# Kernel optimization log

Hardware: AMD Instinct MI355X
Metric: run time of the kernel (lower is better)

Reference implementation:

```python
import jax, jax.numpy as jnp
import numpy as np

D_MODEL = 2048; D_STATE = 128; D_CONV = 4; EXPAND = 2
HEADDIM = 64; NGROUPS = 1; CHUNK = 256
D_INNER = EXPAND * D_MODEL          # 4096
NHEADS = D_INNER // HEADDIM         # 64
HG = NHEADS // NGROUPS              # heads per group
CONV_DIM = D_INNER + 2 * NGROUPS * D_STATE          # 4352
D_IN_PROJ = 2 * D_INNER + 2 * NGROUPS * D_STATE + NHEADS  # 8512
BATCH = 2; SEQLEN = 2048
EPS = 1e-5


def setup_inputs() -> dict:
    ks = jax.random.split(jax.random.key(0), 8)
    u = jax.random.normal(ks[0], (BATCH, SEQLEN, D_MODEL), jnp.float32)
    in_proj_w = jax.random.normal(ks[1], (D_IN_PROJ, D_MODEL), jnp.float32) * D_MODEL ** -0.5
    conv_w = jax.random.normal(ks[2], (CONV_DIM, D_CONV), jnp.float32) * D_CONV ** -0.5
    conv_b = jax.random.normal(ks[3], (CONV_DIM,), jnp.float32) * 0.1
    # dt_bias init exactly as in the module: inv softplus of dt ~ U(log(1e-3), log(1e-1))
    dt = jnp.exp(jax.random.uniform(ks[4], (NHEADS,), jnp.float32)
                 * (np.float32(np.log(0.1)) - np.float32(np.log(0.001))) + np.float32(np.log(0.001)))
    dt = jnp.clip(dt, 1e-4, None)
    dt_bias = dt + jnp.log(-jnp.expm1(-dt))
    A_log = jnp.log(jax.random.uniform(ks[5], (NHEADS,), jnp.float32, minval=1.0, maxval=16.0))
    D_skip = jnp.ones((NHEADS,), jnp.float32)
    norm_w = jnp.ones((D_INNER,), jnp.float32)
    out_proj_w = jax.random.normal(ks[6], (D_MODEL, D_INNER), jnp.float32) * D_INNER ** -0.5
    return dict(u=u, in_proj_w=in_proj_w, conv_w=conv_w, conv_b=conv_b,
                dt_bias=dt_bias, A_log=A_log, D_skip=D_skip,
                norm_w=norm_w, out_proj_w=out_proj_w)


def _mamba2(u, in_proj_w, conv_w, conv_b, dt_bias, A_log, D_skip, norm_w, out_proj_w):
    b, l, _ = u.shape
    nc = l // CHUNK
    zxbcdt = u @ in_proj_w.T                                   # (b,l,d_in_proj)
    z = zxbcdt[..., :D_INNER]                                  # gate
    xBC = zxbcdt[..., D_INNER:D_INNER + CONV_DIM]
    dt = jax.nn.softplus(zxbcdt[..., D_INNER + CONV_DIM:] + dt_bias)  # (b,l,h)
    # causal depthwise conv1d (padding d_conv-1, truncated to seqlen) + SiLU
    xp = jnp.pad(xBC, ((0, 0), (D_CONV - 1, 0), (0, 0)))
    conv = conv_b + sum(conv_w[:, k] * xp[:, k:k + l, :] for k in range(D_CONV))
    xBC = jax.nn.silu(conv)
    x = xBC[..., :D_INNER].reshape(b, l, NHEADS, HEADDIM)
    Bm = xBC[..., D_INNER:D_INNER + NGROUPS * D_STATE].reshape(b, l, NGROUPS, D_STATE)
    Cm = xBC[..., D_INNER + NGROUPS * D_STATE:].reshape(b, l, NGROUPS, D_STATE)
    A = -jnp.exp(A_log)                                        # (h,)
    # ---- SSD chunked scan ----
    xc = x.reshape(b, nc, CHUNK, NGROUPS, HG, HEADDIM)         # (b,c,s,g,H,p)
    dtc = dt.reshape(b, nc, CHUNK, NGROUPS, HG)                # (b,c,s,g,H)
    Bc = Bm.reshape(b, nc, CHUNK, NGROUPS, D_STATE)            # (b,c,s,g,n)
    Cc = Cm.reshape(b, nc, CHUNK, NGROUPS, D_STATE)
    dA = jnp.transpose(dtc * A.reshape(NGROUPS, HG), (0, 3, 4, 1, 2))  # (b,g,H,c,s)
    dA_cs = jnp.cumsum(dA, axis=-1)                            # (b,g,H,c,s)
    # intra-chunk: L[i,j] = exp(sum_{j<k<=i} dA_k), lower-triangular (diag=1)
    seg = dA_cs[..., :, None] - dA_cs[..., None, :]            # (b,g,H,c,l,s)
    tri = jnp.tril(jnp.ones((CHUNK, CHUNK), bool))
    Lmat = jnp.where(tri, jnp.exp(seg), 0.0)
    xdt = xc * dtc[..., None]                                  # (b,c,s,g,H,p)
    CB = jnp.einsum('bclgn,bcsgn->bcgls', Cc, Bc)
    Y_diag = jnp.einsum('bcgls,bgHcls,bcsgHp->bclgHp', CB, Lmat, xdt)
    # chunk states and inter-chunk recurrence
    decay_states = jnp.exp(dA_cs[..., -1:] - dA_cs)            # (b,g,H,c,s)
    states = jnp.einsum('bcsgn,bgHcs,bcsgHp->bcgHpn', Bc, decay_states, xdt)
    chunk_decay = jnp.exp(dA_cs[..., -1])                      # (b,g,H,c)

    def step(carry, inp):
        st, dec = inp
        return carry * dec[..., None, None] + st, carry

    _, prev = jax.lax.scan(step, jnp.zeros_like(states[:, 0]),
                           (jnp.moveaxis(states, 1, 0), jnp.moveaxis(chunk_decay, -1, 0)))
    prev = jnp.moveaxis(prev, 0, 1)                            # (b,c,g,H,p,n) state entering chunk
    Y_off = jnp.einsum('bclgn,bcgHpn,bgHcl->bclgHp', Cc, prev, jnp.exp(dA_cs))
    y = (Y_diag + Y_off).reshape(b, l, NHEADS, HEADDIM) + x * D_skip[None, None, :, None]
    y = y.reshape(b, l, D_INNER)
    # gated RMSNorm: gate first (norm_before_gate=False), groupwise rms (ngroups=1 -> full)
    y = y * jax.nn.silu(z)
    yg = y.reshape(b, l, NGROUPS, D_INNER // NGROUPS)
    yg = yg * jax.lax.rsqrt(jnp.mean(yg * yg, axis=-1, keepdims=True) + EPS)
    y = yg.reshape(b, l, D_INNER) * norm_w
    return y @ out_proj_w.T                                    # (b,l,d_model)


def reference(u, in_proj_w, conv_w, conv_b, dt_bias, A_log, D_skip, norm_w, out_proj_w):
    return _mamba2(u, in_proj_w, conv_w, conv_b, dt_bias, A_log, D_skip, norm_w, out_proj_w)
```

## Files before the change

kernel.cpp:

```cpp
#include <hip/hip_runtime.h>
#include <hip/hip_bf16.h>


#define D_MODEL   2048
#define D_STATE   128
#define HEADDIM   64
#define CHUNK     256
#define D_INNER   4096
#define NHEADS    64
#define CONV_DIM  4352
#define D_IN_PROJ 8512
#define SEQLEN    2048
#define NC        8
#define ROWSTOT   4096
#define NPAD      8576
#define RMS_EPS   1e-5f

#define OFF_WIN   0ull
#define OFF_XBF   0ull
#define OFF_PREV  0ull
#define OFF_WOUT  16777216ull
#define OFF_UBF   35127296ull
#define OFF_DTV   35127296ull
#define OFF_DACS  36175872ull
#define OFF_BBF   37224448ull
#define OFF_CBF   38273024ull
#define OFF_CB    39321600ull
#define OFF_BT    43515904ull
#define OFF_XBC   51904512ull
#define OFF_STATE 51904512ull
#define OFF_ZBF   87556096ull
#define OFF_DTRAW 121110528ull
#define OFF_YBUF  121110528ull
#define WS_NEEDED 154664960ull

typedef __hip_bfloat16 bf16;
typedef __bf16 bfrag8 __attribute__((ext_vector_type(8)));
typedef float  f32x4v __attribute__((ext_vector_type(4)));

__device__ __forceinline__ f32x4v mfma16(bfrag8 a, bfrag8 b, f32x4v c) {
  return __builtin_amdgcn_mfma_f32_16x16x32_bf16(a, b, c, 0, 0, 0);
}

__device__ __forceinline__ void gload_lds16(const void* g, void* l) {
  __builtin_amdgcn_global_load_lds((const __attribute__((address_space(1))) void*)g,
                                   (__attribute__((address_space(3))) void*)l, 16, 0, 0);
}

__device__ __forceinline__ bf16 f2b(float x) { return __float2bfloat16(x); }
__device__ __forceinline__ float b2f(bf16 x) { return __bfloat162float(x); }
__device__ __forceinline__ float siluf(float x) { return x / (1.f + __expf(-x)); }

__global__ __launch_bounds__(256) void cast_kernel(const float* __restrict__ in,
                                                   bf16* __restrict__ out, long n4) {
  long i = (long)blockIdx.x * 256 + threadIdx.x;
  if (i >= n4) return;
  float4 v = ((const float4*)in)[i];
  bf16* o = out + i * 4;
  o[0] = f2b(v.x); o[1] = f2b(v.y); o[2] = f2b(v.z); o[3] = f2b(v.w);
}

__global__ __launch_bounds__(256) void cast_pad_kernel(const float* __restrict__ in,
                                                       bf16* __restrict__ out) {
  long i = (long)blockIdx.x * 256 + threadIdx.x;
  long e = i * 4;
  if (e >= (long)NPAD * D_MODEL) return;
  long row = e / D_MODEL;
  bf16* o = out + e;
  if (row < D_IN_PROJ) {
    float4 v = *(const float4*)(in + e);
    o[0] = f2b(v.x); o[1] = f2b(v.y); o[2] = f2b(v.z); o[3] = f2b(v.w);
  } else {
    bf16 z = f2b(0.f);
    o[0] = z; o[1] = z; o[2] = z; o[3] = z;
  }
}

#define STAGE64(SRC, DST, base_row, Kld, kt)                                     \
  {                                                                              \
    int ci = (j * 4 + w) * 64 + lane;                               \
    int half = ci >> 9, cj = ci & 511;                                           \
    int r = cj >> 2, ko = half * 32 + (cj & 3) * 8;                              \
    gload_lds16(SRC + (base_row + r) * (long)Kld + kt + ko,                      \
                (char*)DST + (j * 4 + w) * 1024);                                \
  }

__global__ __launch_bounds__(256) void gemm1_kernel(const bf16* __restrict__ A,
                                                    const bf16* __restrict__ B,
                                                    bf16* __restrict__ zb,
                                                    bf16* __restrict__ xbc,
                                                    float* __restrict__ dtraw) {
  int pid = blockIdx.x;
  int t = pid & 127, s = pid >> 7;
  int sm = s / 9, sn = s % 9;
  int tm = sm * 16 + (t & 15);
  int tn = sn * 8 + (t >> 4);
  if (tn >= 67) return;
  long row0 = (long)tm * 128, col0 = (long)tn * 128;

  __shared__ __align__(16) bf16 As[2 * 128 * 32];
  __shared__ __align__(16) bf16 Bs[2 * 128 * 32];
  int tid = threadIdx.x, lane = tid & 63, w = tid >> 6;
  int wr = w >> 1, wc = w & 1, r16 = lane & 15, q = lane >> 4;
  const int K = D_MODEL;
  f32x4v zero4 = {0.f, 0.f, 0.f, 0.f};
  f32x4v acc[4][4];
#pragma unroll
  for (int i = 0; i < 4; ++i)
#pragma unroll
    for (int j = 0; j < 4; ++j) acc[i][j] = zero4;

  for (int kt = 0; kt < K; kt += 64) {
    __syncthreads();
#pragma unroll
    for (int j = 0; j < 4; ++j) {
      STAGE64(A, As, row0, K, kt);
      STAGE64(B, Bs, col0, K, kt);
    }
    __syncthreads();
#pragma unroll
    for (int ks = 0; ks < 2; ++ks) {
      const bf16* Ab = As + ks * 4096;
      const bf16* Bb = Bs + ks * 4096;
      bfrag8 af[4], bfv[4];
#pragma unroll
      for (int i = 0; i < 4; ++i) af[i]  = *(const bfrag8*)(Ab + (wr * 64 + i * 16 + r16) * 32 + q * 8);
#pragma unroll
      for (int i = 0; i < 4; ++i) bfv[i] = *(const bfrag8*)(Bb + (wc * 64 + i * 16 + r16) * 32 + q * 8);
#pragma unroll
      for (int i = 0; i < 4; ++i)
#pragma unroll
        for (int j = 0; j < 4; ++j) acc[i][j] = mfma16(af[i], bfv[j], acc[i][j]);
    }
  }
#pragma unroll
  for (int i = 0; i < 4; ++i)
#pragma unroll
    for (int j = 0; j < 4; ++j) {
      long col = col0 + wc * 64 + j * 16 + r16;
#pragma unroll
      for (int r = 0; r < 4; ++r) {
        long row = row0 + wr * 64 + i * 16 + q * 4 + r;
        float v = acc[i][j][r];
        if (col < D_INNER)                       zb[row * D_INNER + col] = f2b(v);
        else if (col < D_INNER + CONV_DIM)       xbc[row * CONV_DIM + (col - D_INNER)] = f2b(v);
        else if (col < D_IN_PROJ)                dtraw[row * NHEADS + (col - D_INNER - CONV_DIM)] = v;
      }
    }
}

__global__ __launch_bounds__(256) void gemm2_kernel(const bf16* __restrict__ A,
                                                    const bf16* __restrict__ B,
                                                    float* __restrict__ C) {
  int pid = blockIdx.x;
  int t = pid & 63, s = pid >> 6;
  int sm = s >> 1, sn = s & 1;
  int tm = sm * 8 + (t & 7);
  int tn = sn * 8 + (t >> 3);
  long row0 = (long)tm * 128, col0 = (long)tn * 128;

  __shared__ __align__(16) bf16 As[2 * 128 * 32];
  __shared__ __align__(16) bf16 Bs[2 * 128 * 32];
  int tid = threadIdx.x, lane = tid & 63, w = tid >> 6;
  int wr = w >> 1, wc = w & 1, r16 = lane & 15, q = lane >> 4;
  const int K = D_INNER, ldc = D_MODEL;
  f32x4v zero4 = {0.f, 0.f, 0.f, 0.f};
  f32x4v acc[4][4];
#pragma unroll
  for (int i = 0; i < 4; ++i)
#pragma unroll
    for (int j = 0; j < 4; ++j) acc[i][j] = zero4;

  for (int kt = 0; kt < K; kt += 64) {
    __syncthreads();
#pragma unroll
    for (int j = 0; j < 4; ++j) {
      STAGE64(A, As, row0, K, kt);
      STAGE64(B, Bs, col0, K, kt);
    }
    __syncthreads();
#pragma unroll
    for (int ks = 0; ks < 2; ++ks) {
      const bf16* Ab = As + ks * 4096;
      const bf16* Bb = Bs + ks * 4096;
      bfrag8 af[4], bfv[4];
#pragma unroll
      for (int i = 0; i < 4; ++i) af[i]  = *(const bfrag8*)(Ab + (wr * 64 + i * 16 + r16) * 32 + q * 8);
#pragma unroll
      for (int i = 0; i < 4; ++i) bfv[i] = *(const bfrag8*)(Bb + (wc * 64 + i * 16 + r16) * 32 + q * 8);
#pragma unroll
      for (int i = 0; i < 4; ++i)
#pragma unroll
        for (int j = 0; j < 4; ++j) acc[i][j] = mfma16(af[i], bfv[j], acc[i][j]);
    }
  }
#pragma unroll
  for (int i = 0; i < 4; ++i)
#pragma unroll
    for (int j = 0; j < 4; ++j)
#pragma unroll
      for (int r = 0; r < 4; ++r) {
        long row = row0 + wr * 64 + i * 16 + q * 4 + r;
        long col = col0 + wc * 64 + j * 16 + r16;
        C[row * ldc + col] = acc[i][j][r];
      }
}

__global__ __launch_bounds__(256) void dt_scan_kernel(const float* __restrict__ dtraw,
    const float* __restrict__ dt_bias, const float* __restrict__ A_log,
    float* __restrict__ dtv_buf, float* __restrict__ dacs_buf) {
  int blk = blockIdx.x;
  int c = blk & 7, h = (blk >> 3) & 63, b = blk >> 9;
  int s = threadIdx.x, lane = s & 63, w = s >> 6;
  long row = (long)b * SEQLEN + c * CHUNK + s;
  float raw = dtraw[row * NHEADS + h] + dt_bias[h];
  float dtv = fmaxf(raw, 0.f) + log1pf(__expf(-fabsf(raw)));
  float A = -__expf(A_log[h]);
  float x = dtv * A;
#pragma unroll
  for (int off = 1; off < 64; off <<= 1) {
    float y = __shfl_up(x, off);
    if (lane >= off) x += y;
  }
  __shared__ __align__(16) float wsum[4];
  if (lane == 63) wsum[w] = x;
  __syncthreads();
  float pre = 0.f;
#pragma unroll
  for (int i = 0; i < 4; ++i) pre += (i < w) ? wsum[i] : 0.f;
  long o = ((long)(b * NHEADS + h) * NC + c) * CHUNK + s;
  dtv_buf[o] = dtv;
  dacs_buf[o] = x + pre;
}

__global__ __launch_bounds__(256) void conv_kernel(const bf16* __restrict__ xbc,
    const float* __restrict__ conv_w, const float* __restrict__ conv_b,
    bf16* __restrict__ xo, bf16* __restrict__ Bo, bf16* __restrict__ Co,
    bf16* __restrict__ BT) {
  int cidx = blockIdx.x * 256 + threadIdx.x;
  int l0 = blockIdx.y * 8, b = blockIdx.z;
  float4 wv = *(const float4*)(conv_w + cidx * 4);
  float bias = conv_b[cidx];
  const bf16* base = xbc + (long)b * SEQLEN * CONV_DIM + cidx;
  float win[11];
#pragma unroll
  for (int k = 0; k < 11; ++k) {
    int ls = l0 - 3 + k;
    win[k] = (ls >= 0) ? b2f(base[(long)ls * CONV_DIM]) : 0.f;
  }
  int cgrp = (cidx < D_INNER) ? 0 : ((cidx < D_INNER + D_STATE) ? 1 : 2);
  int n = cidx - D_INNER;
  int n2 = cidx - D_INNER - D_STATE;
  int cch = l0 >> 8;
#pragma unroll
  for (int j = 0; j < 8; ++j) {
    float acc = bias + wv.x * win[j] + wv.y * win[j + 1] + wv.z * win[j + 2] + wv.w * win[j + 3];
    bf16 o = f2b(siluf(acc));
    int l = l0 + j;
    long rowo = (long)b * SEQLEN + l;
    if (cgrp == 0) {
      xo[rowo * D_INNER + cidx] = o;
    } else if (cgrp == 1) {
      Bo[rowo * D_STATE + n] = o;
      BT[(((long)b * NC + cch) * D_STATE + n) * CHUNK + (l & 255)] = o;
    } else {
      Co[rowo * D_STATE + n2] = o;
    }
  }
}

__global__ __launch_bounds__(256) void cb_kernel(const bf16* __restrict__ Cg,
                                                 const bf16* __restrict__ Bg,
                                                 float* __restrict__ CB) {
  int blk = blockIdx.x;
  int stile = blk & 3, bc = blk >> 2;
  int c = bc & 7, b = bc >> 3;
  int tid = threadIdx.x, lane = tid & 63, w = tid >> 6, r16 = lane & 15, q = lane >> 4;
  const bf16* Cb = Cg + ((long)b * SEQLEN + c * CHUNK) * D_STATE;
  const bf16* Bb = Bg + ((long)b * SEQLEN + c * CHUNK) * D_STATE;
  bfrag8 af[4][4];
#pragma unroll
  for (int lt = 0; lt < 4; ++lt)
#pragma unroll
    for (int kk = 0; kk < 4; ++kk)
      af[lt][kk] = *(const bfrag8*)(Cb + (long)(w * 64 + lt * 16 + r16) * D_STATE + kk * 32 + q * 8);
  float* CBb = CB + (long)bc * CHUNK * CHUNK;
  f32x4v zero4 = {0.f, 0.f, 0.f, 0.f};
  for (int st = stile * 4; st < stile * 4 + 4; ++st) {
    f32x4v acc[4] = {zero4, zero4, zero4, zero4};
#pragma unroll
    for (int kk = 0; kk < 4; ++kk) {
      bfrag8 bfv = *(const bfrag8*)(Bb + (long)(st * 16 + r16) * D_STATE + kk * 32 + q * 8);
#pragma unroll
      for (int lt = 0; lt < 4; ++lt) acc[lt] = mfma16(af[lt][kk], bfv, acc[lt]);
    }
#pragma unroll
    for (int lt = 0; lt < 4; ++lt)
#pragma unroll
      for (int r = 0; r < 4; ++r)
        CBb[(long)(w * 64 + lt * 16 + q * 4 + r) * CHUNK + st * 16 + r16] = acc[lt][r];
  }
}

__global__ __launch_bounds__(256) void ssm_diag_kernel(
    const bf16* __restrict__ xg, const bf16* __restrict__ BT,
    const float* __restrict__ CB, const float* __restrict__ dtv_buf,
    const float* __restrict__ dacs_buf, const float* __restrict__ Dskip,
    bf16* __restrict__ ybuf, float* __restrict__ states) {
  int blk = blockIdx.x;
  int h = blk & 63, cc = (blk >> 6) & 7, b = blk >> 9;
  int tid = threadIdx.x, lane = tid & 63, w = tid >> 6, r16 = lane & 15, q = lane >> 4;

  __shared__ __align__(16) __bf16 xT[HEADDIM][264];
  __shared__ __align__(16) float cs_s[CHUNK];
  __shared__ __align__(16) float dt_s[CHUNK];
  __shared__ __align__(16) float w_s[CHUNK];

  long hco = ((long)(b * NHEADS + h) * NC + cc) * CHUNK;
  cs_s[tid] = dacs_buf[hco + tid];
  dt_s[tid] = dtv_buf[hco + tid];
  __syncthreads();
  float cl_last = cs_s[CHUNK - 1];
  w_s[tid] = __expf(cl_last - cs_s[tid]) * dt_s[tid];

  const __bf16* xbase = (const __bf16*)(xg + ((long)b * SEQLEN + cc * CHUNK) * D_INNER + h * HEADDIM);
#pragma unroll
  for (int it = 0; it < 8; ++it) {
    int e = it * 256 + tid;
    int s = e >> 3, p0 = (e & 7) * 8;
    bfrag8 xv = *(const bfrag8*)(xbase + (long)s * D_INNER + p0);
#pragma unroll
    for (int j = 0; j < 8; ++j) xT[p0 + j][s] = xv[j];
  }
  __syncthreads();

  const float* CBchunk = CB + (long)(b * NC + cc) * CHUNK * CHUNK;
  const __bf16* BTc = (const __bf16*)(BT + (((long)b * NC + cc) * D_STATE) * CHUNK);
  f32x4v zero4 = {0.f, 0.f, 0.f, 0.f};
  f32x4v accY[4][4], accS[2][4];
#pragma unroll
  for (int i = 0; i < 4; ++i)
#pragma unroll
    for (int j = 0; j < 4; ++j) accY[i][j] = zero4;
#pragma unroll
  for (int i = 0; i < 2; ++i)
#pragma unroll
    for (int j = 0; j < 4; ++j) accS[i][j] = zero4;

  int l_row[4];
  const float* CBrow[4];
#pragma unroll
  for (int lt = 0; lt < 4; ++lt) {
    l_row[lt] = w * 64 + lt * 16 + r16;
    CBrow[lt] = CBchunk + (long)l_row[lt] * CHUNK;
  }

#pragma unroll 2
  for (int ks = 0; ks < 8; ++ks) {
    int s0 = ks * 32 + q * 8;
    float4 cs0 = *(const float4*)(cs_s + s0);
    float4 cs1 = *(const float4*)(cs_s + s0 + 4);
    float4 dt0 = *(const float4*)(dt_s + s0);
    float4 dt1 = *(const float4*)(dt_s + s0 + 4);
    float4 w0  = *(const float4*)(w_s + s0);
    float4 w1  = *(const float4*)(w_s + s0 + 4);
    float csv[8] = {cs0.x, cs0.y, cs0.z, cs0.w, cs1.x, cs1.y, cs1.z, cs1.w};
    float dtv8[8] = {dt0.x, dt0.y, dt0.z, dt0.w, dt1.x, dt1.y, dt1.z, dt1.w};
    float wv8[8]  = {w0.x, w0.y, w0.z, w0.w, w1.x, w1.y, w1.z, w1.w};

    bfrag8 xf[4];
#pragma unroll
    for (int pt = 0; pt < 4; ++pt) xf[pt] = *(const bfrag8*)(&xT[pt * 16 + r16][s0]);

#pragma unroll
    for (int lt = 0; lt < 4; ++lt) {
      int l = l_row[lt];
      float cs_l = cs_s[l];
      float4 cb0 = *(const float4*)(CBrow[lt] + s0);
      float4 cb1 = *(const float4*)(CBrow[lt] + s0 + 4);
      float cbv[8] = {cb0.x, cb0.y, cb0.z, cb0.w, cb1.x, cb1.y, cb1.z, cb1.w};
      bfrag8 pf;
#pragma unroll
      for (int j = 0; j < 8; ++j) {
        float v = (s0 + j <= l)
                    ? cbv[j] * __expf(fminf(cs_l - csv[j], 0.f)) * dtv8[j]
                    : 0.f;
        pf[j] = (__bf16)v;
      }
#pragma unroll
      for (int pt = 0; pt < 4; ++pt) accY[lt][pt] = mfma16(pf, xf[pt], accY[lt][pt]);
    }

#pragma unroll
    for (int nt = 0; nt < 2; ++nt) {
      int n = w * 32 + nt * 16 + r16;
      bfrag8 braw = *(const bfrag8*)(BTc + (long)n * CHUNK + s0);
      bfrag8 bwf;
#pragma unroll
      for (int j = 0; j < 8; ++j) bwf[j] = (__bf16)((float)braw[j] * wv8[j]);
#pragma unroll
      for (int pt = 0; pt < 4; ++pt) accS[nt][pt] = mfma16(bwf, xf[pt], accS[nt][pt]);
    }
  }

  float dsk = Dskip[h];
  bf16* ybase = ybuf + ((long)b * SEQLEN + cc * CHUNK) * D_INNER + h * HEADDIM;
#pragma unroll
  for (int lt = 0; lt < 4; ++lt)
#pragma unroll
    for (int pt = 0; pt < 4; ++pt)
#pragma unroll
      for (int r = 0; r < 4; ++r) {
        int lrow = w * 64 + lt * 16 + q * 4 + r;
        int pcol = pt * 16 + r16;
        ybase[(long)lrow * D_INNER + pcol] = f2b(accY[lt][pt][r] + (float)xT[pcol][lrow] * dsk);
      }
  float* sbase = states + (long)blk * (HEADDIM * D_STATE);
#pragma unroll
  for (int nt = 0; nt < 2; ++nt)
#pragma unroll
    for (int pt = 0; pt < 4; ++pt)
#pragma unroll
      for (int r = 0; r < 4; ++r)
        sbase[(long)(pt * 16 + r16) * D_STATE + w * 32 + nt * 16 + q * 4 + r] = accS[nt][pt][r];
}

__global__ __launch_bounds__(256) void state_scan_kernel(const float* __restrict__ states,
    const float* __restrict__ dacs, bf16* __restrict__ prevb) {
  int gid = blockIdx.x;
  int et = gid & 31, bh = gid >> 5;
  int h = bh & 63, b = bh >> 6;
  int e = et * 256 + threadIdx.x;
  float dec[NC];
#pragma unroll
  for (int c = 0; c < NC; ++c)
    dec[c] = __expf(dacs[((long)(b * NHEADS + h) * NC + c) * CHUNK + (CHUNK - 1)]);
  float carry = 0.f;
#pragma unroll
  for (int c = 0; c < NC; ++c) {
    long off = ((long)((b * NC + c) * NHEADS + h)) * (HEADDIM * D_STATE) + e;
    prevb[off] = f2b(carry);
    carry = carry * dec[c] + states[off];
  }
}

__global__ __launch_bounds__(256) void yoff_kernel(const bf16* __restrict__ Cg,
    const bf16* __restrict__ prevb, const float* __restrict__ dacs,
    bf16* __restrict__ ybuf) {
  int blk = blockIdx.x;
  int h = blk & 63, cc = (blk >> 6) & 7, b = blk >> 9;
  int tid = threadIdx.x, lane = tid & 63, w = tid >> 6, r16 = lane & 15, q = lane >> 4;
  __shared__ __align__(16) float cs_s[CHUNK];
  cs_s[tid] = dacs[((long)(b * NHEADS + h) * NC + cc) * CHUNK + tid];
  __syncthreads();
  const bf16* Cb = Cg + ((long)b * SEQLEN + cc * CHUNK) * D_STATE;
  const bf16* Pb = prevb + (long)blk * (HEADDIM * D_STATE);
  f32x4v zero4 = {0.f, 0.f, 0.f, 0.f};
  f32x4v acc[4][4];
#pragma unroll
  for (int i = 0; i < 4; ++i)
#pragma unroll
    for (int j = 0; j < 4; ++j) acc[i][j] = zero4;
#pragma unroll
  for (int kk = 0; kk < 4; ++kk) {
    bfrag8 bv[4];
#pragma unroll
    for (int pt = 0; pt < 4; ++pt)
      bv[pt] = *(const bfrag8*)(Pb + (long)(pt * 16 + r16) * D_STATE + kk * 32 + q * 8);
#pragma unroll
    for (int lt = 0; lt < 4; ++lt) {
      bfrag8 av = *(const bfrag8*)(Cb + (long)(w * 64 + lt * 16 + r16) * D_STATE + kk * 32 + q * 8);
#pragma unroll
      for (int pt = 0; pt < 4; ++pt) acc[lt][pt] = mfma16(av, bv[pt], acc[lt][pt]);
    }
  }
  bf16* ybase = ybuf + ((long)b * SEQLEN + cc * CHUNK) * D_INNER + h * HEADDIM;
#pragma unroll
  for (int lt = 0; lt < 4; ++lt)
#pragma unroll
    for (int pt = 0; pt < 4; ++pt)
#pragma unroll
      for (int r = 0; r < 4; ++r) {
        int lrow = w * 64 + lt * 16 + q * 4 + r;
        float ef = __expf(cs_s[lrow]);
        bf16* p = ybase + (long)lrow * D_INNER + pt * 16 + r16;
        *p = f2b(b2f(*p) + acc[lt][pt][r] * ef);
      }
}

__global__ __launch_bounds__(256) void gate_norm_kernel(bf16* __restrict__ ybuf,
    const bf16* __restrict__ zb, const float* __restrict__ norm_w) {
  int row = blockIdx.x, tid = threadIdx.x;
  bf16* y = ybuf + (long)row * D_INNER;
  const bf16* z = zb + (long)row * D_INNER;
  float v[16];
  float ss = 0.f;
#pragma unroll
  for (int i = 0; i < 2; ++i) {
    int e = tid * 16 + i * 8;
    bfrag8 yv = *(const bfrag8*)(y + e);
    bfrag8 zv = *(const bfrag8*)(z + e);
#pragma unroll
    for (int j = 0; j < 8; ++j) {
      float a = (float)yv[j] * siluf((float)zv[j]);
      v[i * 8 + j] = a;
      ss += a * a;
    }
  }
#pragma unroll
  for (int off = 32; off > 0; off >>= 1) ss += __shfl_down(ss, off);
  __shared__ __align__(16) float red[4];
  int lane = tid & 63, w = tid >> 6;
  if (lane == 0) red[w] = ss;
  __syncthreads();
  float tot = red[0] + red[1] + red[2] + red[3];
  float scale = rsqrtf(tot * (1.f / D_INNER) + RMS_EPS);
#pragma unroll
  for (int i = 0; i < 2; ++i) {
    int e = tid * 16 + i * 8;
    float4 w0 = *(const float4*)(norm_w + e);
    float4 w1 = *(const float4*)(norm_w + e + 4);
    bfrag8 o;
    o[0] = (__bf16)(v[i * 8 + 0] * scale * w0.x);
    o[1] = (__bf16)(v[i * 8 + 1] * scale * w0.y);
    o[2] = (__bf16)(v[i * 8 + 2] * scale * w0.z);
    o[3] = (__bf16)(v[i * 8 + 3] * scale * w0.w);
    o[4] = (__bf16)(v[i * 8 + 4] * scale * w1.x);
    o[5] = (__bf16)(v[i * 8 + 5] * scale * w1.y);
    o[6] = (__bf16)(v[i * 8 + 6] * scale * w1.z);
    o[7] = (__bf16)(v[i * 8 + 7] * scale * w1.w);
    *(bfrag8*)(y + e) = o;
  }
}

extern "C" void kernel_launch(void* const* d_in, const int* in_sizes, int n_in,
                              void* d_out, int out_size, void* d_ws, size_t ws_size,
                              hipStream_t stream) {
  if (ws_size < WS_NEEDED) return;

  const float* u       = (const float*)d_in[0];
  const float* w_in    = (const float*)d_in[1];
  const float* conv_w  = (const float*)d_in[2];
  const float* conv_b  = (const float*)d_in[3];
  const float* dt_bias = (const float*)d_in[4];
  const float* A_log   = (const float*)d_in[5];
  const float* Dskip   = (const float*)d_in[6];
  const float* norm_w  = (const float*)d_in[7];
  const float* w_out   = (const float*)d_in[8];
  float* out = (float*)d_out;

  char* ws = (char*)d_ws;
  bf16*  win_bf  = (bf16*)(ws + OFF_WIN);
  bf16*  x_bf    = (bf16*)(ws + OFF_XBF);
  bf16*  prevb   = (bf16*)(ws + OFF_PREV);
  bf16*  wout_bf = (bf16*)(ws + OFF_WOUT);
  bf16*  u_bf    = (bf16*)(ws + OFF_UBF);
  float* dtv     = (float*)(ws + OFF_DTV);
  float* dacs    = (float*)(ws + OFF_DACS);
  bf16*  B_bf    = (bf16*)(ws + OFF_BBF);
  bf16*  C_bf    = (bf16*)(ws + OFF_CBF);
  float* CBb     = (float*)(ws + OFF_CB);
  bf16*  BT_bf   = (bf16*)(ws + OFF_BT);
  bf16*  xbc_bf  = (bf16*)(ws + OFF_XBC);
  float* states  = (float*)(ws + OFF_STATE);
  bf16*  z_bf    = (bf16*)(ws + OFF_ZBF);
  float* dt_raw  = (float*)(ws + OFF_DTRAW);
  bf16*  ybuf    = (bf16*)(ws + OFF_YBUF);

  cast_kernel<<<8192, 256, 0, stream>>>(u, u_bf, (long)ROWSTOT * D_MODEL / 4);
  cast_pad_kernel<<<17152, 256, 0, stream>>>(w_in, win_bf);
  gemm1_kernel<<<2304, 256, 0, stream>>>(u_bf, win_bf, z_bf, xbc_bf, dt_raw);
  dt_scan_kernel<<<1024, 256, 0, stream>>>(dt_raw, dt_bias, A_log, dtv, dacs);
  conv_kernel<<<dim3(17, SEQLEN / 8, 2), 256, 0, stream>>>(xbc_bf, conv_w, conv_b, x_bf, B_bf, C_bf, BT_bf);
  cb_kernel<<<64, 256, 0, stream>>>(C_bf, B_bf, CBb);
  ssm_diag_kernel<<<1024, 256, 0, stream>>>(x_bf, BT_bf, CBb, dtv, dacs, Dskip, ybuf, states);
  state_scan_kernel<<<4096, 256, 0, stream>>>(states, dacs, prevb);
  yoff_kernel<<<1024, 256, 0, stream>>>(C_bf, prevb, dacs, ybuf);
  cast_kernel<<<8192, 256, 0, stream>>>(w_out, wout_bf, (long)D_MODEL * D_INNER / 4);
  gate_norm_kernel<<<ROWSTOT, 256, 0, stream>>>(ybuf, z_bf, norm_w);
  gemm2_kernel<<<512, 256, 0, stream>>>(ybuf, wout_bf, out);
}
```

Baseline: 631.3 us.

## Enlarge gemm1 tile to 256x128, remap blocks per XCD, merge cast kernels

gemm1 now uses 512-thread blocks computing 256x128 output tiles with 8 waves, so each B tile is reused across twice as many rows. Both GEMMs remap block ids so consecutive blocks on the same XCD share neighbouring tiles, aiming for better L2 reuse. The two input cast kernels are merged into one launch. The larger tile doubles LDS use per block and halves the block count, which may reduce occupancy.

```diff
diff --git a/kernel.cpp b/kernel.cpp
--- a/kernel.cpp
+++ b/kernel.cpp
@@ -34,6 +34,9 @@
 #define OFF_YBUF  121110528ull
 #define WS_NEEDED 154664960ull
 
+#define N4_U    2097152l
+#define N4_WIN  4390912l
+
 typedef __hip_bfloat16 bf16;
 typedef __bf16 bfrag8 __attribute__((ext_vector_type(8)));
 typedef float  f32x4v __attribute__((ext_vector_type(4)));
@@ -50,6 +53,28 @@
 __device__ __forceinline__ bf16 f2b(float x) { return __float2bfloat16(x); }
 __device__ __forceinline__ float b2f(bf16 x) { return __bfloat162float(x); }
 __device__ __forceinline__ float siluf(float x) { return x / (1.f + __expf(-x)); }
+
+__global__ __launch_bounds__(256) void cast_all_kernel(const float* __restrict__ u,
+    const float* __restrict__ w_in,
+    bf16* __restrict__ u_bf, bf16* __restrict__ win_bf) {
+  long i = (long)blockIdx.x * 256 + threadIdx.x;
+  if (i < N4_U) {
+    float4 v = ((const float4*)u)[i];
+    bf16* o = u_bf + i * 4;
+    o[0] = f2b(v.x); o[1] = f2b(v.y); o[2] = f2b(v.z); o[3] = f2b(v.w);
+  } else if (i < N4_U + N4_WIN) {
+    long e = (i - N4_U) * 4;
+    long row = e / D_MODEL;
+    bf16* o = win_bf + e;
+    if (row < D_IN_PROJ) {
+      float4 v = *(const float4*)(w_in + e);
+      o[0] = f2b(v.x); o[1] = f2b(v.y); o[2] = f2b(v.z); o[3] = f2b(v.w);
+    } else {
+      bf16 z = f2b(0.f);
+      o[0] = z; o[1] = z; o[2] = z; o[3] = z;
+    }
+  }
+}
 
 __global__ __launch_bounds__(256) void cast_kernel(const float* __restrict__ in,
                                                    bf16* __restrict__ out, long n4) {
@@ -60,45 +85,21 @@
   o[0] = f2b(v.x); o[1] = f2b(v.y); o[2] = f2b(v.z); o[3] = f2b(v.w);
 }
 
-__global__ __launch_bounds__(256) void cast_pad_kernel(const float* __restrict__ in,
-                                                       bf16* __restrict__ out) {
-  long i = (long)blockIdx.x * 256 + threadIdx.x;
-  long e = i * 4;
-  if (e >= (long)NPAD * D_MODEL) return;
-  long row = e / D_MODEL;
-  bf16* o = out + e;
-  if (row < D_IN_PROJ) {
-    float4 v = *(const float4*)(in + e);
-    o[0] = f2b(v.x); o[1] = f2b(v.y); o[2] = f2b(v.z); o[3] = f2b(v.w);
-  } else {
-    bf16 z = f2b(0.f);
-    o[0] = z; o[1] = z; o[2] = z; o[3] = z;
-  }
-}
-
-#define STAGE64(SRC, DST, base_row, Kld, kt)                                     \
-  {                                                                              \
-    int ci = (j * 4 + w) * 64 + lane;                               \
-    int half = ci >> 9, cj = ci & 511;                                           \
-    int r = cj >> 2, ko = half * 32 + (cj & 3) * 8;                              \
-    gload_lds16(SRC + (base_row + r) * (long)Kld + kt + ko,                      \
-                (char*)DST + (j * 4 + w) * 1024);                                \
-  }
-
-__global__ __launch_bounds__(256) void gemm1_kernel(const bf16* __restrict__ A,
+__global__ __launch_bounds__(512) void gemm1_kernel(const bf16* __restrict__ A,
                                                     const bf16* __restrict__ B,
                                                     bf16* __restrict__ zb,
                                                     bf16* __restrict__ xbc,
                                                     float* __restrict__ dtraw) {
   int pid = blockIdx.x;
-  int t = pid & 127, s = pid >> 7;
+  int t = pid & 63, s = pid >> 6;
   int sm = s / 9, sn = s % 9;
-  int tm = sm * 16 + (t & 15);
-  int tn = sn * 8 + (t >> 4);
+  int xcd = t & 7, j8 = t >> 3;
+  int tm = sm * 8 + (xcd >> 1) * 2 + (j8 & 1);
+  int tn = sn * 8 + (xcd & 1) * 4 + (j8 >> 1);
   if (tn >= 67) return;
-  long row0 = (long)tm * 128, col0 = (long)tn * 128;
-
-  __shared__ __align__(16) bf16 As[2 * 128 * 32];
+  long row0 = (long)tm * 256, col0 = (long)tn * 128;
+
+  __shared__ __align__(16) bf16 As[2 * 256 * 32];
   __shared__ __align__(16) bf16 Bs[2 * 128 * 32];
   int tid = threadIdx.x, lane = tid & 63, w = tid >> 6;
   int wr = w >> 1, wc = w & 1, r16 = lane & 15, q = lane >> 4;
@@ -114,13 +115,24 @@
     __syncthreads();
 #pragma unroll
     for (int j = 0; j < 4; ++j) {
-      STAGE64(A, As, row0, K, kt);
-      STAGE64(B, Bs, col0, K, kt);
+      int ci = j * 512 + tid;
+      int half = ci >> 10, cj = ci & 1023;
+      int r = cj >> 2, ko = half * 32 + (cj & 3) * 8;
+      gload_lds16(A + (row0 + r) * (long)K + kt + ko,
+                  (char*)As + j * 8192 + w * 1024);
+    }
+#pragma unroll
+    for (int j = 0; j < 2; ++j) {
+      int ci = j * 512 + tid;
+      int half = ci >> 9, cj = ci & 511;
+      int r = cj >> 2, ko = half * 32 + (cj & 3) * 8;
+      gload_lds16(B + (col0 + r) * (long)K + kt + ko,
+                  (char*)Bs + j * 8192 + w * 1024);
     }
     __syncthreads();
 #pragma unroll
     for (int ks = 0; ks < 2; ++ks) {
-      const bf16* Ab = As + ks * 4096;
+      const bf16* Ab = As + ks * 8192;
       const bf16* Bb = Bs + ks * 4096;
       bfrag8 af[4], bfv[4];
 #pragma unroll
@@ -155,8 +167,9 @@
   int pid = blockIdx.x;
   int t = pid & 63, s = pid >> 6;
   int sm = s >> 1, sn = s & 1;
-  int tm = sm * 8 + (t & 7);
-  int tn = sn * 8 + (t >> 3);
+  int xcd = t & 7, j8 = t >> 3;
+  int tm = sm * 8 + (xcd >> 1) * 2 + (j8 & 1);
+  int tn = sn * 8 + (xcd & 1) * 4 + (j8 >> 1);
   long row0 = (long)tm * 128, col0 = (long)tn * 128;
 
   __shared__ __align__(16) bf16 As[2 * 128 * 32];
@@ -175,8 +188,19 @@
     __syncthreads();
 #pragma unroll
     for (int j = 0; j < 4; ++j) {
-      STAGE64(A, As, row0, K, kt);
-      STAGE64(B, Bs, col0, K, kt);
+      int ci = (j * 4 + w) * 64 + lane;
+      int half = ci >> 9, cj = ci & 511;
+      int r = cj >> 2, ko = half * 32 + (cj & 3) * 8;
+      gload_lds16(A + (row0 + r) * (long)K + kt + ko,
+                  (char*)As + (j * 4 + w) * 1024);
+    }
+#pragma unroll
+    for (int j = 0; j < 4; ++j) {
+      int ci = (j * 4 + w) * 64 + lane;
+      int half = ci >> 9, cj = ci & 511;
+      int r = cj >> 2, ko = half * 32 + (cj & 3) * 8;
+      gload_lds16(B + (col0 + r) * (long)K + kt + ko,
+                  (char*)Bs + (j * 4 + w) * 1024);
     }
     __syncthreads();
 #pragma unroll
@@ -567,9 +591,8 @@
   float* dt_raw  = (float*)(ws + OFF_DTRAW);
   bf16*  ybuf    = (bf16*)(ws + OFF_YBUF);
 
-  cast_kernel<<<8192, 256, 0, stream>>>(u, u_bf, (long)ROWSTOT * D_MODEL / 4);
-  cast_pad_kernel<<<17152, 256, 0, stream>>>(w_in, win_bf);
-  gemm1_kernel<<<2304, 256, 0, stream>>>(u_bf, win_bf, z_bf, xbc_bf, dt_raw);
+  cast_all_kernel<<<25344, 256, 0, stream>>>(u, w_in, u_bf, win_bf);
+  gemm1_kernel<<<1152, 512, 0, stream>>>(u_bf, win_bf, z_bf, xbc_bf, dt_raw);
   dt_scan_kernel<<<1024, 256, 0, stream>>>(dt_raw, dt_bias, A_log, dtv, dacs);
   conv_kernel<<<dim3(17, SEQLEN / 8, 2), 256, 0, stream>>>(xbc_bf, conv_w, conv_b, x_bf, B_bf, C_bf, BT_bf);
   cb_kernel<<<64, 256, 0, stream>>>(C_bf, B_bf, CBb);
```

Result: faster. 590.5 us (-6.4%).
